# Optimization experiments

Hardware: AMD Instinct MI355X
Metric: run time of the kernel (lower is better)

The kernel has to match this reference:

```python
import jax, jax.numpy as jnp
import numpy as np

FLOW_SCALE = 8.0  # typical pixel displacement magnitude


def setup_inputs() -> dict:
    key = jax.random.key(0)
    k1, k2, k3 = jax.random.split(key, 3)
    tenInput = jax.random.normal(k1, (4, 64, 256, 448), dtype=jnp.float32)
    tenFlow = jax.random.normal(k2, (4, 2, 256, 448), dtype=jnp.float32) * FLOW_SCALE
    tenMetric = jax.random.normal(k3, (4, 1, 256, 448), dtype=jnp.float32)
    return {"tenInput": tenInput, "tenFlow": tenFlow, "tenMetric": tenMetric}


def _softsplat_sum(vals, flow):
    # vals: [C1, H, W] augmented input, flow: [2, H, W] (x-disp, y-disp)
    C1, H, W = vals.shape
    gx = jnp.arange(W, dtype=flow.dtype)
    gy = jnp.arange(H, dtype=flow.dtype)
    fltX = gx[None, :] + flow[0]  # [H, W] target x
    fltY = gy[:, None] + flow[1]  # [H, W] target y
    x0 = jnp.floor(fltX)
    y0 = jnp.floor(fltY)
    x1 = x0 + 1.0
    y1 = y0 + 1.0
    # bilinear splat weights for the 4 neighbors
    wNW = (x1 - fltX) * (y1 - fltY)
    wNE = (fltX - x0) * (y1 - fltY)
    wSW = (x1 - fltX) * (fltY - y0)
    wSE = (fltX - x0) * (fltY - y0)
    valsf = vals.reshape(C1, H * W)
    out = jnp.zeros((C1, H * W), dtype=vals.dtype)
    for xi, yi, w in ((x0, y0, wNW), (x1, y0, wNE), (x0, y1, wSW), (x1, y1, wSE)):
        xi_i = xi.astype(jnp.int32)
        yi_i = yi.astype(jnp.int32)
        valid = (xi_i >= 0) & (xi_i < W) & (yi_i >= 0) & (yi_i < H)
        idx = jnp.where(valid, yi_i * W + xi_i, 0).reshape(-1)   # [H*W]
        wv = jnp.where(valid, w, 0.0).reshape(-1)                # [H*W]
        out = out.at[:, idx].add(valsf * wv[None, :])
    return out.reshape(C1, H, W)


def reference(tenInput, tenFlow, tenMetric):
    # strType == 'softmax': splat [input*exp(metric), exp(metric)], then normalize
    m = jnp.exp(tenMetric)                                 # [B,1,H,W]
    aug = jnp.concatenate([tenInput * m, m], axis=1)       # [B,C+1,H,W]
    out = jax.vmap(_softsplat_sum)(aug, tenFlow)           # [B,C+1,H,W]
    norm = out[:, -1:, :, :]
    norm = jnp.where(norm == 0.0, jnp.ones_like(norm), norm)
    return out[:, :-1, :, :] / norm
```

## Files before the change

### kernel.cpp

```cpp
#include <hip/hip_runtime.h>

constexpr int N = 4;
constexpr int C = 64;
constexpr int H = 256;
constexpr int W = 448;
constexpr int HW = H * W;

constexpr int BSX = 4;
constexpr int BSY = 4;
constexpr int BW_ = W / BSX;
constexpr int BH_ = H / BSY;
constexpr int BINS_PB = BW_ * BH_;
constexpr int BINS = N * BINS_PB;


__device__ __forceinline__ int binsOf(int x0, int y0, int bins[4]) {
    const int x1 = x0 + 1, y1 = y0 + 1;
    int n = 0;
    int bxA = -2, bxB = -2, byA = -2, byB = -2;
    if ((unsigned)x0 < (unsigned)W) bxA = x0 >> 2;
    if ((unsigned)x1 < (unsigned)W) { const int t = x1 >> 2; if (t != bxA) bxB = t; }
    if ((unsigned)y0 < (unsigned)H) byA = y0 >> 2;
    if ((unsigned)y1 < (unsigned)H) { const int t = y1 >> 2; if (t != byA) byB = t; }
    if (byA >= 0) {
        if (bxA >= 0) bins[n++] = byA * BW_ + bxA;
        if (bxB >= 0) bins[n++] = byA * BW_ + bxB;
    }
    if (byB >= 0) {
        if (bxA >= 0) bins[n++] = byB * BW_ + bxA;
        if (bxB >= 0) bins[n++] = byB * BW_ + bxB;
    }
    return n;
}

__global__ __launch_bounds__(1024) void count_kernel(
    const float* __restrict__ flow,
    unsigned* __restrict__ counts)
{
    __shared__ unsigned lcnt[BINS_PB];
    const int tid = threadIdx.x;
    const int idx = blockIdx.x * 1024 + tid;
    const int b = idx / HW;
    const int p = idx - b * HW;
    const int y = p / W;
    const int x = p - y * W;

    for (int i = tid; i < BINS_PB; i += 1024) lcnt[i] = 0;
    __syncthreads();

    const float fx = (float)x + flow[(b * 2 + 0) * HW + p];
    const float fy = (float)y + flow[(b * 2 + 1) * HW + p];
    const int x0 = (int)floorf(fx), y0 = (int)floorf(fy);

    int bn[4];
    const int nb = binsOf(x0, y0, bn);
    for (int i = 0; i < nb; ++i) atomicAdd(&lcnt[bn[i]], 1u);
    __syncthreads();

    for (int i = tid; i < BINS_PB; i += 1024)
        if (lcnt[i]) atomicAdd(&counts[b * BINS_PB + i], lcnt[i]);
}

__global__ __launch_bounds__(1024) void scan_kernel(
    const unsigned* __restrict__ counts,
    unsigned* __restrict__ segstart,
    unsigned capE)
{
    __shared__ unsigned lsum[1024];
    const int tid = threadIdx.x;
    constexpr int VPT = BINS / 1024;
    unsigned v[VPT];
    unsigned s = 0;
#pragma unroll
    for (int i = 0; i < VPT; ++i) { v[i] = counts[tid * VPT + i]; s += v[i]; }
    lsum[tid] = s;
    __syncthreads();
    for (int off = 1; off < 1024; off <<= 1) {
        const unsigned t = (tid >= off) ? lsum[tid - off] : 0u;
        __syncthreads();
        lsum[tid] += t;
        __syncthreads();
    }
    unsigned run = lsum[tid] - s;
#pragma unroll
    for (int i = 0; i < VPT; ++i) {
        segstart[tid * VPT + i] = run < capE ? run : capE;
        run += v[i];
    }
    if (tid == 1023) segstart[BINS] = run < capE ? run : capE;
}

__global__ __launch_bounds__(1024) void fill2_kernel(
    const float* __restrict__ flow,
    const float* __restrict__ metric,
    const unsigned* __restrict__ segstart,
    unsigned* __restrict__ cursor,
    float4* __restrict__ recs,
    unsigned capE)
{
    const int tid = threadIdx.x;
    const int idx = blockIdx.x * 1024 + tid;
    const int b = idx / HW;
    const int p = idx - b * HW;
    const int y = p / W;
    const int x = p - y * W;

    const float fx = (float)x + flow[(b * 2 + 0) * HW + p];
    const float fy = (float)y + flow[(b * 2 + 1) * HW + p];
    const float m  = __expf(metric[b * HW + p]);
    const int x0 = (int)floorf(fx), y0 = (int)floorf(fy);

    int bn[4];
    const int nb = binsOf(x0, y0, bn);
    const float4 rec = make_float4(fx, fy, m, __int_as_float(p));
    const int tb = b * BINS_PB;
    for (int i = 0; i < nb; ++i) {
        const unsigned off = atomicAdd(&cursor[tb + bn[i]], 1u);
        const unsigned slot = segstart[tb + bn[i]] + off;
        if (slot < capE) recs[slot] = rec;
    }
}

__global__ __launch_bounds__(256) void augT_kernel(
    const float* __restrict__ input,
    const float* __restrict__ metric,
    float* __restrict__ aug)
{
    __shared__ float s_val[128][65];
    __shared__ float s_m[128];

    const int tid = threadIdx.x;
    const int blockPix = blockIdx.x * 128;
    const int b = blockPix / HW;
    const int pb = blockPix - b * HW;

    if (tid < 128)
        s_m[tid] = __expf(metric[b * HW + pb + tid]);

    {
        const int sp = tid & 127;
        const int sc = tid >> 7;
        const float* ib = input + (size_t)b * C * HW + pb + sp;
#pragma unroll
        for (int c = 0; c < 32; ++c) {
            const int ch = 2 * c + sc;
            s_val[sp][ch] = ib[(size_t)ch * HW];
        }
    }
    __syncthreads();

    const int wv = tid >> 6, ln = tid & 63;
    float* abase = aug + ((size_t)b * HW + pb) * 64;
#pragma unroll
    for (int it = 0; it < 32; ++it) {
        const int j = (wv << 5) + it;
        abase[(size_t)j * 64 + ln] = s_val[j][ln] * s_m[j];
    }
}

#define ROW4(J, WGT) do { const float tv_ = v0 * (WGT);                   \
    _Pragma("unroll")                                                     \
    for (int i_ = 0; i_ < 4; ++i_)                                        \
        acc[(J) * 4 + i_] = fmaf(tv_, axx[i_], acc[(J) * 4 + i_]);        \
} while (0)

__global__ __launch_bounds__(64, 2) void gather6(
    const float4* __restrict__ recs,
    const float* __restrict__ aug,
    const unsigned* __restrict__ segstart,
    float* __restrict__ out)
{
    __shared__ float st[16][65];

    const int lane = threadIdx.x;

    const int nwg = gridDim.x;
    const int bid = blockIdx.x;
    const int g   = (bid & 7) * (nwg >> 3) + (bid >> 3);

    const int b   = g / BINS_PB;
    const int bin = g - b * BINS_PB;
    const int by  = bin / BW_;
    const int bx  = bin - by * BW_;
    const int qx0 = bx * BSX;
    const int qy0 = by * BSY;

    const float Xp = (float)(qx0 + (lane & 3));
    const float Yp = (float)(qy0 + ((lane >> 2) & 3));

    float acc[16];
#pragma unroll
    for (int i = 0; i < 16; ++i) acc[i] = 0.0f;
    float nrm = 0.0f;

    const int start = (int)segstart[g];
    const int end   = (int)segstart[g + 1];
    const float* ab = aug + (size_t)b * HW * 64;

    const float4 Z = make_float4(0.0f, 0.0f, 0.0f, __int_as_float(0));
    float4 r0 = Z, r1 = Z, r2 = Z;
    float v0 = 0.0f, v1 = 0.0f;
    if (start + 0 < end) r0 = recs[start + 0];
    if (start + 1 < end) r1 = recs[start + 1];
    if (start + 2 < end) r2 = recs[start + 2];
    if (start + 0 < end) {
        const int p0 = __builtin_amdgcn_readfirstlane(__float_as_int(r0.w));
        v0 = ab[(size_t)p0 * 64 + lane];
    }
    if (start + 1 < end) {
        const int p1 = __builtin_amdgcn_readfirstlane(__float_as_int(r1.w));
        v1 = ab[(size_t)p1 * 64 + lane];
    }

    for (int e = start; e < end; ++e) {
        float4 r3 = Z;
        if (e + 3 < end) r3 = recs[e + 3];
        float v2 = 0.0f;
        if (e + 2 < end) {
            const int p2 = __builtin_amdgcn_readfirstlane(__float_as_int(r2.w));
            v2 = ab[(size_t)p2 * 64 + lane];
        }

        const float fxl = r0.x - (float)qx0;
        const float fyl = r0.y - (float)qy0;
        float axx[4];
#pragma unroll
        for (int i = 0; i < 4; ++i)
            axx[i] = fmaxf(1.0f - fabsf(fxl - (float)i), 0.0f);

        const float fyf = floorf(fyl);
        const int   j0  = (int)fyf;
        const float fr  = fyl - fyf;
        const float wA  = 1.0f - fr, wB = fr;
        switch (j0) {
            case -1: ROW4(0, wB); break;
            case 0:  ROW4(0, wA); ROW4(1, wB); break;
            case 1:  ROW4(1, wA); ROW4(2, wB); break;
            case 2:  ROW4(2, wA); ROW4(3, wB); break;
            default: ROW4(3, wA); break;
        }

        const float axn = fmaxf(1.0f - fabsf(r0.x - Xp), 0.0f);
        const float ayn = fmaxf(1.0f - fabsf(r0.y - Yp), 0.0f);
        nrm = fmaf(r0.z, axn * ayn, nrm);

        r0 = r1; r1 = r2; r2 = r3; v0 = v1; v1 = v2;
    }

    const float inv = (nrm == 0.0f) ? 1.0f : (1.0f / nrm);

#pragma unroll
    for (int px = 0; px < 16; ++px)
        st[px][lane] = acc[px];
    asm volatile("s_waitcnt lgkmcnt(0)" ::: "memory");

    float* ob = out + (size_t)b * C * HW;
    const int pl = lane & 15;
    const int cs = lane >> 4;
    const int ooff = (qy0 + ((pl >> 2) & 3)) * W + qx0 + (pl & 3);
#pragma unroll
    for (int it = 0; it < 16; ++it) {
        const int c = it * 4 + cs;
        ob[(size_t)c * HW + ooff] = st[pl][c] * inv;
    }
}

__global__ __launch_bounds__(256) void splat_nhwc(
    const float* __restrict__ input,
    const float* __restrict__ flow,
    const float* __restrict__ metric,
    float* __restrict__ scr,
    float* __restrict__ norm)
{
    __shared__ float s_val[128][65];
    __shared__ float s_fx[128], s_fy[128], s_m[128];

    const int tid = threadIdx.x;
    const int nwg = gridDim.x;
    const int bid = blockIdx.x;
    const int swz = (bid & 7) * (nwg >> 3) + (bid >> 3);

    const int blockPix = swz * 128;
    const int b = blockPix / HW;
    const int pb = blockPix - b * HW;

    if (tid < 128) {
        const int p = pb + tid;
        const int y = p / W;
        const int x = p - y * W;
        s_fx[tid] = (float)x + flow[(b * 2 + 0) * HW + p];
        s_fy[tid] = (float)y + flow[(b * 2 + 1) * HW + p];
        s_m[tid]  = __expf(metric[b * HW + p]);
    }
    {
        const int sp = tid & 127;
        const int sc = tid >> 7;
        const float* ib = input + (size_t)b * C * HW + pb + sp;
#pragma unroll
        for (int c = 0; c < 32; ++c) {
            const int ch = 2 * c + sc;
            s_val[sp][ch] = ib[(size_t)ch * HW];
        }
    }
    __syncthreads();

    const int wave = tid >> 6;
    const int lane = tid & 63;
    float* __restrict__ sb = scr + (size_t)b * HW * 64;
    float* __restrict__ nb = norm + b * HW;

    for (int k = 0; k < 32; ++k) {
        const int j = (wave << 5) | k;
        const float fx = s_fx[j], fy = s_fy[j], m = s_m[j];
        const float v = s_val[j][lane] * m;

        const float x0f = floorf(fx), y0f = floorf(fy);
        const int x0 = (int)x0f, y0 = (int)y0f;
        const int x1 = x0 + 1,   y1 = y0 + 1;
        const float wx1 = fx - x0f, wx0 = 1.0f - wx1;
        const float wy1 = fy - y0f, wy0 = 1.0f - wy1;

        const bool vx0 = (x0 >= 0) & (x0 < W);
        const bool vx1 = (x1 >= 0) & (x1 < W);
        const bool vy0 = (y0 >= 0) & (y0 < H);
        const bool vy1 = (y1 >= 0) & (y1 < H);

        if (vx0 & vy0) {
            const float w = wx0 * wy0; const int t = y0 * W + x0;
            atomicAdd(sb + (size_t)t * 64 + lane, v * w);
            if (lane == 0) atomicAdd(nb + t, m * w);
        }
        if (vx1 & vy0) {
            const float w = wx1 * wy0; const int t = y0 * W + x1;
            atomicAdd(sb + (size_t)t * 64 + lane, v * w);
            if (lane == 0) atomicAdd(nb + t, m * w);
        }
        if (vx0 & vy1) {
            const float w = wx0 * wy1; const int t = y1 * W + x0;
            atomicAdd(sb + (size_t)t * 64 + lane, v * w);
            if (lane == 0) atomicAdd(nb + t, m * w);
        }
        if (vx1 & vy1) {
            const float w = wx1 * wy1; const int t = y1 * W + x1;
            atomicAdd(sb + (size_t)t * 64 + lane, v * w);
            if (lane == 0) atomicAdd(nb + t, m * w);
        }
    }
}

__global__ __launch_bounds__(256) void untranspose_norm(
    const float* __restrict__ scr,
    const float* __restrict__ norm,
    float* __restrict__ out)
{
    __shared__ float s_t[64][65];
    __shared__ float s_inv[64];

    const int tid = threadIdx.x;
    const int strips = HW / 64;
    const int b = blockIdx.x / strips;
    const int pblk = (blockIdx.x - b * strips) * 64;

    if (tid < 64) {
        float n = norm[b * HW + pblk + tid];
        s_inv[tid] = (n == 0.0f) ? 1.0f : (1.0f / n);
    }
    const float* sb = scr + ((size_t)b * HW + pblk) * 64;
#pragma unroll
    for (int r = 0; r < 16; ++r) {
        const int pr = r * 4 + (tid >> 6);
        const int c  = tid & 63;
        s_t[pr][c] = sb[(size_t)pr * 64 + c];
    }
    __syncthreads();

    float* ob = out + (size_t)b * C * HW + pblk;
#pragma unroll
    for (int r = 0; r < 16; ++r) {
        const int c   = r * 4 + (tid >> 6);
        const int pix = tid & 63;
        ob[(size_t)c * HW + pix] = s_t[pix][c] * s_inv[pix];
    }
}

__global__ void splat_kernel(const float* __restrict__ input,
                             const float* __restrict__ flow,
                             const float* __restrict__ metric,
                             float* __restrict__ out,
                             float* __restrict__ norm)
{
    int idx = blockIdx.x * blockDim.x + threadIdx.x;
    if (idx >= N * HW) return;
    int b = idx / HW;
    int p = idx - b * HW;
    int y = p / W;
    int x = p - y * W;

    float fx = (float)x + flow[(b * 2 + 0) * HW + p];
    float fy = (float)y + flow[(b * 2 + 1) * HW + p];
    float m  = __expf(metric[b * HW + p]);

    float x0f = floorf(fx), y0f = floorf(fy);
    int x0 = (int)x0f, y0 = (int)y0f;
    int x1 = x0 + 1,   y1 = y0 + 1;
    float wx1 = fx - x0f, wx0 = 1.0f - wx1;
    float wy1 = fy - y0f, wy0 = 1.0f - wy1;

    bool vx0 = (x0 >= 0) & (x0 < W);
    bool vx1 = (x1 >= 0) & (x1 < W);
    bool vy0 = (y0 >= 0) & (y0 < H);
    bool vy1 = (y1 >= 0) & (y1 < H);

    bool vNW = vx0 & vy0, vNE = vx1 & vy0, vSW = vx0 & vy1, vSE = vx1 & vy1;
    float wNW = wx0 * wy0, wNE = wx1 * wy0, wSW = wx0 * wy1, wSE = wx1 * wy1;
    int iNW = y0 * W + x0, iNE = y0 * W + x1, iSW = y1 * W + x0, iSE = y1 * W + x1;

    {
        float* nb = norm + b * HW;
        if (vNW) atomicAdd(nb + iNW, m * wNW);
        if (vNE) atomicAdd(nb + iNE, m * wNE);
        if (vSW) atomicAdd(nb + iSW, m * wSW);
        if (vSE) atomicAdd(nb + iSE, m * wSE);
    }

    const float* ib = input + (size_t)b * C * HW + p;
    float* ob = out + (size_t)b * C * HW;
#pragma unroll 4
    for (int c = 0; c < C; ++c) {
        float v = ib[(size_t)c * HW] * m;
        float* oc = ob + (size_t)c * HW;
        if (vNW) atomicAdd(oc + iNW, v * wNW);
        if (vNE) atomicAdd(oc + iNE, v * wNE);
        if (vSW) atomicAdd(oc + iSW, v * wSW);
        if (vSE) atomicAdd(oc + iSE, v * wSE);
    }
}

__global__ void norm_kernel(float* __restrict__ out,
                            const float* __restrict__ norm)
{
    int idx = blockIdx.x * blockDim.x + threadIdx.x;
    int total = N * C * HW / 4;
    if (idx >= total) return;

    int pixq = idx % (HW / 4);
    int bc   = idx / (HW / 4);
    int b    = bc / C;

    const float4* np4 = (const float4*)(norm + (size_t)b * HW);
    float4 n = np4[pixq];
    n.x = (n.x == 0.0f) ? 1.0f : n.x;
    n.y = (n.y == 0.0f) ? 1.0f : n.y;
    n.z = (n.z == 0.0f) ? 1.0f : n.z;
    n.w = (n.w == 0.0f) ? 1.0f : n.w;

    float4* o4 = (float4*)out;
    float4 v = o4[idx];
    v.x /= n.x; v.y /= n.y; v.z /= n.z; v.w /= n.w;
    o4[idx] = v;
}

extern "C" void kernel_launch(void* const* d_in, const int* in_sizes, int n_in,
                              void* d_out, int out_size, void* d_ws, size_t ws_size,
                              hipStream_t stream)
{
    const float* input  = (const float*)d_in[0];
    const float* flow   = (const float*)d_in[1];
    const float* metric = (const float*)d_in[2];
    float* out = (float*)d_out;

    const size_t augBytes  = (size_t)N * HW * 64 * sizeof(float);
    const size_t metaBytes = ((size_t)BINS * 2 + BINS + 1) * sizeof(unsigned);

    const size_t capFull = (size_t)4 * N * HW;
    const size_t cap2x   = (size_t)2 * N * HW;

    auto need = [&](size_t capE) {
        return augBytes + capE * sizeof(float4) + metaBytes;
    };
    const size_t need_mid = augBytes + (size_t)N * HW * sizeof(float);

    size_t capE = 0;
    if      (ws_size >= need(capFull)) capE = capFull;
    else if (ws_size >= need(cap2x))   capE = cap2x;

    if (capE) {
        float*    aug      = (float*)d_ws;
        float4*   recs     = (float4*)((char*)d_ws + augBytes);
        unsigned* counts   = (unsigned*)(recs + capE);
        unsigned* cursor   = counts + BINS;
        unsigned* segstart = cursor + BINS;

        hipMemsetAsync(counts, 0, 2 * BINS * sizeof(unsigned), stream);
        count_kernel<<<N * HW / 1024, 1024, 0, stream>>>(flow, counts);
        scan_kernel<<<1, 1024, 0, stream>>>(counts, segstart, (unsigned)capE);
        fill2_kernel<<<N * HW / 1024, 1024, 0, stream>>>(flow, metric, segstart,
                                                         cursor, recs, (unsigned)capE);
        augT_kernel<<<N * HW / 128, 256, 0, stream>>>(input, metric, aug);
        gather6<<<BINS, 64, 0, stream>>>(recs, aug, segstart, out);
    } else if (ws_size >= need_mid) {
        float* scr  = (float*)d_ws;
        float* norm = scr + (size_t)N * HW * 64;
        hipMemsetAsync(scr, 0, need_mid, stream);

        splat_nhwc<<<N * HW / 128, 256, 0, stream>>>(input, flow, metric, scr, norm);
        untranspose_norm<<<N * (HW / 64), 256, 0, stream>>>(scr, norm, out);
    } else {
        float* norm = (float*)d_ws;
        hipMemsetAsync(out,  0, (size_t)N * C * HW * sizeof(float), stream);
        hipMemsetAsync(norm, 0, (size_t)N * HW * sizeof(float), stream);

        splat_kernel<<<(N * HW + 255) / 256, 256, 0, stream>>>(input, flow, metric, out, norm);
        int total = N * C * HW / 4;
        norm_kernel<<<(total + 255) / 256, 256, 0, stream>>>(out, norm);
    }
}
```

Before: 388.0 us.

## Fuse bin counting into aug transpose and gather four bins per workgroup

The separate count kernel is removed. Bin counting now happens inside the aug-transpose kernel, which already reads flow and metric, so one launch and one flow pass go away. It uses global atomics directly instead of block-local shared histograms, which may add atomic contention. The gather kernel now processes four horizontally adjacent bins per 256-thread workgroup, so output stores cover 16 contiguous pixels per row and coalesce better, at the cost of a block-wide barrier.

```diff
diff --git a/kernel.cpp b/kernel.cpp
--- a/kernel.cpp
+++ b/kernel.cpp
@@ -12,6 +12,7 @@
 constexpr int BH_ = H / BSY;
 constexpr int BINS_PB = BW_ * BH_;
 constexpr int BINS = N * BINS_PB;
+constexpr int GRPS_PB = BINS_PB / 4;
 
 
 __device__ __forceinline__ int binsOf(int x0, int y0, int bins[4]) {
@@ -33,34 +34,6 @@
     return n;
 }
 
-__global__ __launch_bounds__(1024) void count_kernel(
-    const float* __restrict__ flow,
-    unsigned* __restrict__ counts)
-{
-    __shared__ unsigned lcnt[BINS_PB];
-    const int tid = threadIdx.x;
-    const int idx = blockIdx.x * 1024 + tid;
-    const int b = idx / HW;
-    const int p = idx - b * HW;
-    const int y = p / W;
-    const int x = p - y * W;
-
-    for (int i = tid; i < BINS_PB; i += 1024) lcnt[i] = 0;
-    __syncthreads();
-
-    const float fx = (float)x + flow[(b * 2 + 0) * HW + p];
-    const float fy = (float)y + flow[(b * 2 + 1) * HW + p];
-    const int x0 = (int)floorf(fx), y0 = (int)floorf(fy);
-
-    int bn[4];
-    const int nb = binsOf(x0, y0, bn);
-    for (int i = 0; i < nb; ++i) atomicAdd(&lcnt[bn[i]], 1u);
-    __syncthreads();
-
-    for (int i = tid; i < BINS_PB; i += 1024)
-        if (lcnt[i]) atomicAdd(&counts[b * BINS_PB + i], lcnt[i]);
-}
-
 __global__ __launch_bounds__(1024) void scan_kernel(
     const unsigned* __restrict__ counts,
     unsigned* __restrict__ segstart,
@@ -121,10 +94,12 @@
     }
 }
 
-__global__ __launch_bounds__(256) void augT_kernel(
+__global__ __launch_bounds__(256) void augTC_kernel(
     const float* __restrict__ input,
+    const float* __restrict__ flow,
     const float* __restrict__ metric,
-    float* __restrict__ aug)
+    float* __restrict__ aug,
+    unsigned* __restrict__ counts)
 {
     __shared__ float s_val[128][65];
     __shared__ float s_m[128];
@@ -134,8 +109,20 @@
     const int b = blockPix / HW;
     const int pb = blockPix - b * HW;
 
-    if (tid < 128)
-        s_m[tid] = __expf(metric[b * HW + pb + tid]);
+    if (tid < 128) {
+        const int p = pb + tid;
+        const int y = p / W;
+        const int x = p - y * W;
+        const float fx = (float)x + flow[(b * 2 + 0) * HW + p];
+        const float fy = (float)y + flow[(b * 2 + 1) * HW + p];
+        s_m[tid] = __expf(metric[b * HW + p]);
+
+        const int x0 = (int)floorf(fx), y0 = (int)floorf(fy);
+        int bn[4];
+        const int nb = binsOf(x0, y0, bn);
+        const int tb = b * BINS_PB;
+        for (int i = 0; i < nb; ++i) atomicAdd(&counts[tb + bn[i]], 1u);
+    }
 
     {
         const int sp = tid & 127;
@@ -164,26 +151,31 @@
         acc[(J) * 4 + i_] = fmaf(tv_, axx[i_], acc[(J) * 4 + i_]);        \
 } while (0)
 
-__global__ __launch_bounds__(64, 2) void gather6(
+__global__ __launch_bounds__(256, 2) void gather7(
     const float4* __restrict__ recs,
     const float* __restrict__ aug,
     const unsigned* __restrict__ segstart,
     float* __restrict__ out)
 {
-    __shared__ float st[16][65];
-
-    const int lane = threadIdx.x;
+    __shared__ float st[4][16][65];
+    __shared__ float s_inv[4][16];
+
+    const int tid  = threadIdx.x;
+    const int wq   = tid >> 6;
+    const int lane = tid & 63;
 
     const int nwg = gridDim.x;
     const int bid = blockIdx.x;
-    const int g   = (bid & 7) * (nwg >> 3) + (bid >> 3);
-
-    const int b   = g / BINS_PB;
-    const int bin = g - b * BINS_PB;
-    const int by  = bin / BW_;
-    const int bx  = bin - by * BW_;
-    const int qx0 = bx * BSX;
-    const int qy0 = by * BSY;
+    const int gg  = (bid & 7) * (nwg >> 3) + (bid >> 3);
+
+    const int b    = gg / GRPS_PB;
+    const int rem  = gg - b * GRPS_PB;
+    const int by   = rem / (BW_ / 4);
+    const int kx   = rem - by * (BW_ / 4);
+    const int qy0  = by * BSY;
+    const int qx0g = kx * 16;
+    const int qx0  = qx0g + wq * BSX;
+    const int g    = b * BINS_PB + by * BW_ + kx * 4 + wq;
 
     const float Xp = (float)(qx0 + (lane & 3));
     const float Yp = (float)(qy0 + ((lane >> 2) & 3));
@@ -248,20 +240,24 @@
     }
 
     const float inv = (nrm == 0.0f) ? 1.0f : (1.0f / nrm);
-
 #pragma unroll
     for (int px = 0; px < 16; ++px)
-        st[px][lane] = acc[px];
-    asm volatile("s_waitcnt lgkmcnt(0)" ::: "memory");
+        st[wq][px][lane] = acc[px];
+    if (lane < 16) s_inv[wq][lane] = inv;
+    __syncthreads();
 
     float* ob = out + (size_t)b * C * HW;
-    const int pl = lane & 15;
-    const int cs = lane >> 4;
-    const int ooff = (qy0 + ((pl >> 2) & 3)) * W + qx0 + (pl & 3);
+    const int px  = tid & 15;
+    const int sub = tid >> 4;
+    const int binl = px >> 2;
 #pragma unroll
     for (int it = 0; it < 16; ++it) {
-        const int c = it * 4 + cs;
-        ob[(size_t)c * HW + ooff] = st[pl][c] * inv;
+        const int k   = it * 16 + sub;
+        const int c   = k >> 2;
+        const int row = k & 3;
+        const int pl  = row * 4 + (px & 3);
+        ob[(size_t)c * HW + (qy0 + row) * W + qx0g + px] =
+            st[binl][pl][c] * s_inv[binl][pl];
     }
 }
 
@@ -492,12 +488,12 @@
         unsigned* segstart = cursor + BINS;
 
         hipMemsetAsync(counts, 0, 2 * BINS * sizeof(unsigned), stream);
-        count_kernel<<<N * HW / 1024, 1024, 0, stream>>>(flow, counts);
+        augTC_kernel<<<N * HW / 128, 256, 0, stream>>>(input, flow, metric,
+                                                       aug, counts);
         scan_kernel<<<1, 1024, 0, stream>>>(counts, segstart, (unsigned)capE);
         fill2_kernel<<<N * HW / 1024, 1024, 0, stream>>>(flow, metric, segstart,
                                                          cursor, recs, (unsigned)capE);
-        augT_kernel<<<N * HW / 128, 256, 0, stream>>>(input, metric, aug);
-        gather6<<<BINS, 64, 0, stream>>>(recs, aug, segstart, out);
+        gather7<<<BINS / 4, 256, 0, stream>>>(recs, aug, segstart, out);
     } else if (ws_size >= need_mid) {
         float* scr  = (float*)d_ws;
         float* norm = scr + (size_t)N * HW * 64;
```

Result: faster. 363.4 us (-6.3%).
